# Optimization experiments

Measured on AMD Instinct MI355X. Metric: run time of the kernel, lower is better.

Reference implementation:

```python
import jax, jax.numpy as jnp
import numpy as np

N = 50000
E = 800000
IN_C = 64
HID = 64
HEADS = 4
NUM_GRAPHS = 64
NEG_SLOPE = 0.2


def setup_inputs() -> dict:
    key = jax.random.key(0)
    ks = jax.random.split(key, 16)
    x = jax.random.normal(ks[0], (N, IN_C), dtype=jnp.float32)
    edge_index = jax.random.randint(ks[1], (2, E), 0, N, dtype=jnp.int64)
    batch = jnp.sort(jax.random.randint(ks[2], (N,), 0, NUM_GRAPHS, dtype=jnp.int64))
    s = lambda *sh: 1.0 / np.sqrt(sh[0])
    # conv1: in -> HID per head, concat -> HEADS*HID
    W1 = jax.random.normal(ks[3], (IN_C, HEADS * HID), dtype=jnp.float32) * s(IN_C)
    a1_src = jax.random.normal(ks[4], (HEADS, HID), dtype=jnp.float32) * s(HID)
    a1_dst = jax.random.normal(ks[5], (HEADS, HID), dtype=jnp.float32) * s(HID)
    b1 = jnp.zeros((HEADS * HID,), dtype=jnp.float32)
    # conv2: HEADS*HID -> HID, single head, no concat
    W2 = jax.random.normal(ks[6], (HEADS * HID, HID), dtype=jnp.float32) * s(HEADS * HID)
    a2_src = jax.random.normal(ks[7], (1, HID), dtype=jnp.float32) * s(HID)
    a2_dst = jax.random.normal(ks[8], (1, HID), dtype=jnp.float32) * s(HID)
    b2 = jnp.zeros((HID,), dtype=jnp.float32)
    # MLP head: HID -> 16 -> 1
    Wh1 = jax.random.normal(ks[9], (HID, 16), dtype=jnp.float32) * s(HID)
    bh1 = jnp.zeros((16,), dtype=jnp.float32)
    Wh2 = jax.random.normal(ks[10], (16, 1), dtype=jnp.float32) * s(16)
    bh2 = jnp.zeros((1,), dtype=jnp.float32)
    return {"x": x, "edge_index": edge_index, "batch": batch,
            "W1": W1, "a1_src": a1_src, "a1_dst": a1_dst, "b1": b1,
            "W2": W2, "a2_src": a2_src, "a2_dst": a2_dst, "b2": b2,
            "Wh1": Wh1, "bh1": bh1, "Wh2": Wh2, "bh2": bh2}


def _gat_conv(x, src, dst, W, a_src, a_dst, b, concat):
    """PyG-style GATConv (eval mode, self-loops already appended)."""
    H, C = a_src.shape
    xp = (x @ W).reshape(-1, H, C)                      # [N,H,C]
    e_s = jnp.einsum('nhc,hc->nh', xp, a_src)            # source contribution
    e_d = jnp.einsum('nhc,hc->nh', xp, a_dst)            # target contribution
    e = jax.nn.leaky_relu(e_s[src] + e_d[dst], NEG_SLOPE)  # [E,H]
    # segment softmax over edges grouped by destination node
    m = jax.ops.segment_max(e, dst, num_segments=N)
    ex = jnp.exp(e - m[dst])
    denom = jax.ops.segment_sum(ex, dst, num_segments=N)
    alpha = ex / denom[dst]                              # [E,H]
    out = jax.ops.segment_sum(alpha[:, :, None] * xp[src], dst, num_segments=N)  # [N,H,C]
    out = out.reshape(-1, H * C) if concat else out.mean(axis=1)
    return out + b


def reference(x, edge_index, batch, W1, a1_src, a1_dst, b1,
              W2, a2_src, a2_dst, b2, Wh1, bh1, Wh2, bh2):
    # add self loops once (GATConv default add_self_loops=True)
    loop = jnp.arange(N, dtype=edge_index.dtype)
    src = jnp.concatenate([edge_index[0], loop])
    dst = jnp.concatenate([edge_index[1], loop])
    h = jax.nn.elu(_gat_conv(x, src, dst, W1, a1_src, a1_dst, b1, concat=True))
    h = _gat_conv(h, src, dst, W2, a2_src, a2_dst, b2, concat=False)
    # global mean pool over graphs
    summed = jax.ops.segment_sum(h, batch, num_segments=NUM_GRAPHS)
    cnt = jax.ops.segment_sum(jnp.ones((N,), h.dtype), batch, num_segments=NUM_GRAPHS)
    pooled = summed / jnp.maximum(cnt, 1.0)[:, None]     # [G,HID]
    z = jax.nn.relu(pooled @ Wh1 + bh1)
    out = jax.nn.sigmoid(z @ Wh2 + bh2)
    return out.squeeze(-1)                               # [G]
```

## Files before the change

### kernel.cpp

```cpp
#include <hip/hip_runtime.h>
#include <math.h>

#define N_NODES 50000
#define N_EDGES 800000
#define EA (N_EDGES + N_NODES)
#define HEADS 4
#define HID 64
#define NG 64
#define NEG_SLOPE 0.2f
#define SCAN_CHUNK 1024
#define NBLK ((N_NODES + SCAN_CHUNK - 1) / SCAN_CHUNK)

typedef _Float16 f16x8 __attribute__((ext_vector_type(8)));
typedef float f32x4 __attribute__((ext_vector_type(4)));
struct h4 { _Float16 a, b, c, d; };

__device__ inline float lrelu(float x) { return x > 0.f ? x : NEG_SLOPE * x; }

__device__ inline f16x8 ldfrag(const _Float16* __restrict__ p, int lq) {
    uint2 lo = *(const uint2*)(p + lq * 4);
    uint2 hi = *(const uint2*)(p + 16 + lq * 4);
    union { uint4 u; f16x8 v; } f;
    f.u = make_uint4(lo.x, lo.y, hi.x, hi.y);
    return f.v;
}

__global__ void k_zero(int* __restrict__ deg, float* __restrict__ pooled,
                       float* __restrict__ cnt)
{
    int i = blockIdx.x * 256 + threadIdx.x;
    int st = gridDim.x * 256;
    for (int j = i; j < N_NODES; j += st) deg[j] = 0;
    if (i < NG * HID) pooled[i] = 0.f;
    if (i < NG) cnt[i] = 0.f;
}

__global__ void k_deg(const int* __restrict__ ei, int* __restrict__ deg)
{
    int e = blockIdx.x * 256 + threadIdx.x;
    if (e >= EA) return;
    int d = (e < N_EDGES) ? ei[N_EDGES + e] : e - N_EDGES;
    atomicAdd(&deg[d], 1);
}

__global__ __launch_bounds__(1024) void k_scan1(const int* __restrict__ deg,
        int* __restrict__ incl, int* __restrict__ blksum)
{
    __shared__ int sd[SCAN_CHUNK];
    int t = threadIdx.x;
    int i = blockIdx.x * SCAN_CHUNK + t;
    sd[t] = (i < N_NODES) ? deg[i] : 0;
    for (int off = 1; off < SCAN_CHUNK; off <<= 1) {
        __syncthreads();
        int u = (t >= off) ? sd[t - off] : 0;
        __syncthreads();
        sd[t] += u;
    }
    if (i < N_NODES) incl[i] = sd[t];
    if (t == SCAN_CHUNK - 1) blksum[blockIdx.x] = sd[t];
}

__global__ __launch_bounds__(256) void k_scan2p(const int* __restrict__ blksum,
        int* __restrict__ blkoff, const float* __restrict__ W1,
        const float* __restrict__ a1s, const float* __restrict__ a1d,
        const float* __restrict__ W2, const float* __restrict__ a2s,
        const float* __restrict__ a2d,
        _Float16* __restrict__ W1P, _Float16* __restrict__ W2P,
        float* __restrict__ va1s, float* __restrict__ va1d,
        float* __restrict__ va2s, float* __restrict__ va2d)
{
    const int t = threadIdx.x;
    if (t == 0) {
        int acc = 0;
        for (int b = 0; b < NBLK; ++b) { blkoff[b] = acc; acc += blksum[b]; }
    }
    for (int i = t; i < 256 * 64; i += 256) {
        int np = i >> 6, k = i & 63;
        W1P[i] = (_Float16)W1[k * 256 + (np & 3) * 64 + (np >> 2)];
    }
    for (int i = t; i < 64 * 256; i += 256) {
        int n = i >> 8, k = i & 255;
        W2P[i] = (_Float16)W2[k * 64 + n];
    }
    {
        int k = t >> 2, h = t & 3;
        float ss = 0.f, sd = 0.f;
        for (int c = 0; c < 64; ++c) {
            float wv = W1[k * 256 + h * 64 + c];
            ss = fmaf(wv, a1s[h * 64 + c], ss);
            sd = fmaf(wv, a1d[h * 64 + c], sd);
        }
        va1s[t] = ss;
        va1d[t] = sd;
    }
    {
        float ss = 0.f, sd = 0.f;
        for (int c = 0; c < 64; ++c) {
            float wv = W2[t * 64 + c];
            ss = fmaf(wv, a2s[c], ss);
            sd = fmaf(wv, a2d[c], sd);
        }
        va2s[t] = ss;
        va2d[t] = sd;
    }
}

__global__ void k_scan3(const int* __restrict__ incl, const int* __restrict__ blkoff,
                        const int* __restrict__ deg, const int* __restrict__ batch,
                        int* __restrict__ rowptr, int* __restrict__ cursor,
                        float* __restrict__ cnt)
{
    int i = blockIdx.x * 256 + threadIdx.x;
    bool act = i < N_NODES;
    if (act) {
        int v = incl[i] + blkoff[i >> 10];
        rowptr[i + 1] = v;
        cursor[i] = v - deg[i];
        if (i == 0) rowptr[0] = 0;
    }
    int g = act ? batch[i] : -1;
    int lane = threadIdx.x & 63;
    int g0 = __shfl(g, 0, 64);
    if (__all(g == g0)) {
        if (lane == 0 && g0 >= 0) atomicAdd(&cnt[g0], 64.f);
    } else if (act) {
        atomicAdd(&cnt[g], 1.f);
    }
}

__global__ void k_fill(const int* __restrict__ ei, int* __restrict__ cursor,
                       int* __restrict__ csr_src)
{
    int e = blockIdx.x * 256 + threadIdx.x;
    if (e >= EA) return;
    int s, d;
    if (e < N_EDGES) { s = ei[e]; d = ei[N_EDGES + e]; }
    else { s = e - N_EDGES; d = s; }
    int pos = atomicAdd(&cursor[d], 1);
    csr_src[pos] = s;
}

__global__ __launch_bounds__(256) void k_gemm1(const float* __restrict__ x,
        const _Float16* __restrict__ W1P, const float* __restrict__ va1s,
        const float* __restrict__ va1d, _Float16* __restrict__ xp1h,
        float* __restrict__ e1s, float* __restrict__ e1d)
{
    const int t = threadIdx.x;
    const int lane = t & 63, w = t >> 6;
    const int l15 = lane & 15, lq = lane >> 4;
    const int m0 = blockIdx.x * 64 + w * 16;
    const int mrow = m0 + l15;
    const int mc = mrow < N_NODES ? mrow : N_NODES - 1;
    const float* xr = x + (size_t)mc * 64;
    float4 x0 = *(const float4*)(xr + lq * 4);
    float4 x1 = *(const float4*)(xr + 16 + lq * 4);
    float4 x2 = *(const float4*)(xr + 32 + lq * 4);
    float4 x3 = *(const float4*)(xr + 48 + lq * 4);
    const float4* vs4 = (const float4*)va1s;
    const float4* vd4 = (const float4*)va1d;
    float4 es = {0,0,0,0}, ed = {0,0,0,0};
    {
        float xv[16] = {x0.x,x0.y,x0.z,x0.w, x1.x,x1.y,x1.z,x1.w,
                        x2.x,x2.y,x2.z,x2.w, x3.x,x3.y,x3.z,x3.w};
        #pragma unroll
        for (int q = 0; q < 4; ++q) {
            int kb = q * 16 + lq * 4;
            #pragma unroll
            for (int j = 0; j < 4; ++j) {
                float v = xv[q * 4 + j];
                float4 a = vs4[kb + j], b = vd4[kb + j];
                es.x = fmaf(v, a.x, es.x); es.y = fmaf(v, a.y, es.y);
                es.z = fmaf(v, a.z, es.z); es.w = fmaf(v, a.w, es.w);
                ed.x = fmaf(v, b.x, ed.x); ed.y = fmaf(v, b.y, ed.y);
                ed.z = fmaf(v, b.z, ed.z); ed.w = fmaf(v, b.w, ed.w);
            }
        }
    }
    #pragma unroll
    for (int off = 16; off <= 32; off <<= 1) {
        es.x += __shfl_down(es.x, off, 64); es.y += __shfl_down(es.y, off, 64);
        es.z += __shfl_down(es.z, off, 64); es.w += __shfl_down(es.w, off, 64);
        ed.x += __shfl_down(ed.x, off, 64); ed.y += __shfl_down(ed.y, off, 64);
        ed.z += __shfl_down(ed.z, off, 64); ed.w += __shfl_down(ed.w, off, 64);
    }
    if (lq == 0 && mrow < N_NODES) {
        ((float4*)e1s)[mrow] = es;
        ((float4*)e1d)[mrow] = ed;
    }
    union { f16x8 v; _Float16 e[8]; } u0, u1;
    u0.e[0]=(_Float16)x0.x; u0.e[1]=(_Float16)x0.y; u0.e[2]=(_Float16)x0.z; u0.e[3]=(_Float16)x0.w;
    u0.e[4]=(_Float16)x1.x; u0.e[5]=(_Float16)x1.y; u0.e[6]=(_Float16)x1.z; u0.e[7]=(_Float16)x1.w;
    u1.e[0]=(_Float16)x2.x; u1.e[1]=(_Float16)x2.y; u1.e[2]=(_Float16)x2.z; u1.e[3]=(_Float16)x2.w;
    u1.e[4]=(_Float16)x3.x; u1.e[5]=(_Float16)x3.y; u1.e[6]=(_Float16)x3.z; u1.e[7]=(_Float16)x3.w;
    #pragma unroll
    for (int ct = 0; ct < 16; ++ct) {
        const _Float16* wrow = W1P + (size_t)(ct * 16 + l15) * 64;
        f16x8 wf0 = ldfrag(wrow, lq);
        f16x8 wf1 = ldfrag(wrow + 32, lq);
        f32x4 acc = {0.f, 0.f, 0.f, 0.f};
        acc = __builtin_amdgcn_mfma_f32_16x16x32_f16(wf0, u0.v, acc, 0, 0, 0);
        acc = __builtin_amdgcn_mfma_f32_16x16x32_f16(wf1, u1.v, acc, 0, 0, 0);
        if (mrow < N_NODES) {
            union { uint2 u2; _Float16 e[4]; } o;
            o.e[0]=(_Float16)acc[0]; o.e[1]=(_Float16)acc[1];
            o.e[2]=(_Float16)acc[2]; o.e[3]=(_Float16)acc[3];
            *(uint2*)(xp1h + (size_t)mrow * 256 + ct * 16 + lq * 4) = o.u2;
        }
    }
}

__global__ __launch_bounds__(256) void k_aggr1(const int* __restrict__ rowptr,
        const int* __restrict__ csr_src, const float* __restrict__ e1s,
        const float* __restrict__ e1d, const _Float16* __restrict__ xp1h,
        const float* __restrict__ b1, const float* __restrict__ va2s,
        const float* __restrict__ va2d, _Float16* __restrict__ h1h,
        float* __restrict__ e2s_o, float* __restrict__ e2d_o)
{
    const int lane = threadIdx.x & 63;
    const int w = __builtin_amdgcn_readfirstlane(threadIdx.x >> 6);
    const int d = blockIdx.x * 4 + w;
    if (d >= N_NODES) return;
    const int beg = rowptr[d], end = rowptr[d + 1];
    const float4 edv = ((const float4*)e1d)[d];
    float a0 = 0.f, a1 = 0.f, a2 = 0.f, a3 = 0.f;
    float d0 = 0.f, d1 = 0.f, d2 = 0.f, d3 = 0.f;
    for (int jb = beg; jb < end; jb += 64) {
        int myj = jb + lane;
        int sv = 0;
        float px = 0.f, py = 0.f, pz = 0.f, pw = 0.f;
        if (myj < end) {
            sv = csr_src[myj];
            float4 q = ((const float4*)e1s)[sv];
            px = __expf(lrelu(q.x + edv.x));
            py = __expf(lrelu(q.y + edv.y));
            pz = __expf(lrelu(q.z + edv.z));
            pw = __expf(lrelu(q.w + edv.w));
        }
        int nj = end - jb; if (nj > 64) nj = 64;
        int njr = (nj + 7) & ~7;
        for (int j = 0; j < njr; j += 8) {
            #pragma unroll
            for (int k = 0; k < 8; ++k) {
                int s = __shfl(sv, j + k, 64);
                float p0 = __shfl(px, j + k, 64);
                float p1 = __shfl(py, j + k, 64);
                float p2 = __shfl(pz, j + k, 64);
                float p3 = __shfl(pw, j + k, 64);
                h4 xv = *(const h4*)(xp1h + (size_t)s * 256 + lane * 4);
                a0 = fmaf(p0, (float)xv.a, a0);
                a1 = fmaf(p1, (float)xv.b, a1);
                a2 = fmaf(p2, (float)xv.c, a2);
                a3 = fmaf(p3, (float)xv.d, a3);
                d0 += p0; d1 += p1; d2 += p2; d3 += p3;
            }
        }
    }
    float acc[4] = {a0 / d0, a1 / d1, a2 / d2, a3 / d3};
    float es = 0.f, edd = 0.f;
    #pragma unroll
    for (int hh = 0; hh < 4; ++hh) {
        float v = acc[hh] + b1[hh * 64 + lane];
        v = v > 0.f ? v : __expf(v) - 1.f;
        h1h[(size_t)d * 256 + hh * 64 + lane] = (_Float16)v;
        es  = fmaf(v, va2s[hh * 64 + lane], es);
        edd = fmaf(v, va2d[hh * 64 + lane], edd);
    }
    #pragma unroll
    for (int off = 32; off > 0; off >>= 1) {
        es += __shfl_down(es, off, 64);
        edd += __shfl_down(edd, off, 64);
    }
    if (lane == 0) { e2s_o[d] = es; e2d_o[d] = edd; }
}

__global__ __launch_bounds__(256) void k_gemm2(const _Float16* __restrict__ h1h,
        const _Float16* __restrict__ W2P, _Float16* __restrict__ xp2h)
{
    const int t = threadIdx.x;
    const int lane = t & 63, w = t >> 6;
    const int l15 = lane & 15, lq = lane >> 4;
    const int m0 = blockIdx.x * 64 + w * 16;
    const int mrow = m0 + l15;
    const _Float16* arow = h1h + (size_t)(m0 + l15) * 256;
    f16x8 af[8];
    #pragma unroll
    for (int ks = 0; ks < 8; ++ks) af[ks] = ldfrag(arow + ks * 32, lq);
    #pragma unroll
    for (int ct = 0; ct < 4; ++ct) {
        const _Float16* wrow = W2P + (size_t)(ct * 16 + l15) * 256;
        f32x4 acc = {0.f, 0.f, 0.f, 0.f};
        #pragma unroll
        for (int ks = 0; ks < 8; ++ks) {
            f16x8 wf = ldfrag(wrow + ks * 32, lq);
            acc = __builtin_amdgcn_mfma_f32_16x16x32_f16(wf, af[ks], acc, 0, 0, 0);
        }
        if (mrow < N_NODES) {
            union { uint2 u2; _Float16 e[4]; } o;
            o.e[0]=(_Float16)acc[0]; o.e[1]=(_Float16)acc[1];
            o.e[2]=(_Float16)acc[2]; o.e[3]=(_Float16)acc[3];
            *(uint2*)(xp2h + (size_t)mrow * 64 + ct * 16 + lq * 4) = o.u2;
        }
    }
}

__global__ __launch_bounds__(256) void k_aggr2(const int* __restrict__ rowptr,
        const int* __restrict__ csr_src, const float* __restrict__ e2s,
        const float* __restrict__ e2d, const _Float16* __restrict__ xp2h,
        const float* __restrict__ b2, const int* __restrict__ batch,
        float* __restrict__ pooled)
{
    const int lane = threadIdx.x & 63;
    const int w = __builtin_amdgcn_readfirstlane(threadIdx.x >> 6);
    const int d = blockIdx.x * 4 + w;
    if (d >= N_NODES) return;
    const int beg = rowptr[d], end = rowptr[d + 1];
    const float edv = e2d[d];
    float acc = 0.f, den = 0.f;
    for (int jb = beg; jb < end; jb += 64) {
        int myj = jb + lane;
        int sv = 0;
        float p = 0.f;
        if (myj < end) {
            sv = csr_src[myj];
            p = __expf(lrelu(e2s[sv] + edv));
        }
        int nj = end - jb; if (nj > 64) nj = 64;
        int njr = (nj + 15) & ~15;
        for (int j = 0; j < njr; j += 16) {
            #pragma unroll
            for (int k = 0; k < 16; ++k) {
                int s = __shfl(sv, j + k, 64);
                float pv = __shfl(p, j + k, 64);
                acc = fmaf(pv, (float)xp2h[(size_t)s * 64 + lane], acc);
                den += pv;
            }
        }
    }
    float val = acc / den + b2[lane];
    int g = batch[d];
    atomicAdd(&pooled[g * 64 + lane], val);
}

__global__ void k_mlp(const float* __restrict__ pooled, const float* __restrict__ cnt,
                      const float* __restrict__ Wh1, const float* __restrict__ bh1,
                      const float* __restrict__ Wh2, const float* __restrict__ bh2,
                      float* __restrict__ out)
{
    int g = threadIdx.x;
    float inv = 1.f / fmaxf(cnt[g], 1.f);
    float p[64];
    #pragma unroll
    for (int c = 0; c < 64; ++c) p[c] = pooled[g * 64 + c] * inv;
    float acc2 = bh2[0];
    for (int j = 0; j < 16; ++j) {
        float z = bh1[j];
        #pragma unroll
        for (int c = 0; c < 64; ++c) z = fmaf(p[c], Wh1[c * 16 + j], z);
        z = fmaxf(z, 0.f);
        acc2 = fmaf(z, Wh2[j], acc2);
    }
    out[g] = 1.f / (1.f + expf(-acc2));
}

extern "C" void kernel_launch(void* const* d_in, const int* in_sizes, int n_in,
                              void* d_out, int out_size, void* d_ws, size_t ws_size,
                              hipStream_t stream)
{
    const float* x      = (const float*)d_in[0];
    const int*   ei     = (const int*)d_in[1];
    const int*   batch  = (const int*)d_in[2];
    const float* W1     = (const float*)d_in[3];
    const float* a1s    = (const float*)d_in[4];
    const float* a1d    = (const float*)d_in[5];
    const float* b1     = (const float*)d_in[6];
    const float* W2     = (const float*)d_in[7];
    const float* a2s    = (const float*)d_in[8];
    const float* a2d    = (const float*)d_in[9];
    const float* b2     = (const float*)d_in[10];
    const float* Wh1    = (const float*)d_in[11];
    const float* bh1    = (const float*)d_in[12];
    const float* Wh2    = (const float*)d_in[13];
    const float* bh2    = (const float*)d_in[14];
    float* out = (float*)d_out;

    float* ws = (float*)d_ws;
    size_t off = 0;
    _Float16* xp1h = (_Float16*)(ws + off); off += (size_t)N_NODES * 128;
    _Float16* h1h  = (_Float16*)(ws + off); off += (size_t)(N_NODES + 64) * 128;
    float* e1s    = ws + off; off += (size_t)N_NODES * 4;
    float* e1d    = ws + off; off += (size_t)N_NODES * 4;
    float* e2s    = ws + off; off += N_NODES;
    float* e2d    = ws + off; off += N_NODES;
    _Float16* xp2h = (_Float16*)(ws + off); off += (size_t)N_NODES * 32;
    _Float16* W1P  = (_Float16*)(ws + off); off += 8192;
    _Float16* W2P  = (_Float16*)(ws + off); off += 8192;
    float* va1s   = ws + off; off += 256;
    float* va1d   = ws + off; off += 256;
    float* va2s   = ws + off; off += 256;
    float* va2d   = ws + off; off += 256;
    float* pooled = ws + off; off += NG * HID;
    float* cnt    = ws + off; off += NG;
    int* rowptr   = (int*)(ws + off); off += N_NODES + 2;
    int* cursor   = (int*)(ws + off); off += N_NODES;
    int* csr_src  = (int*)(ws + off); off += EA;
    int* blksum   = (int*)(ws + off); off += NBLK;
    int* blkoff   = (int*)(ws + off); off += NBLK;
    int* deg  = (int*)h1h;
    int* incl = deg + N_NODES;

    const int BE = (EA + 255) / 256;
    const int BN = (N_NODES + 255) / 256;
    const int BW = (N_NODES + 3) / 4;
    const int BG = (N_NODES + 63) / 64;

    hipLaunchKernelGGL(k_zero,   dim3(64),   dim3(256),  0, stream, deg, pooled, cnt);
    hipLaunchKernelGGL(k_deg,    dim3(BE),   dim3(256),  0, stream, ei, deg);
    hipLaunchKernelGGL(k_scan1,  dim3(NBLK), dim3(1024), 0, stream, deg, incl, blksum);
    hipLaunchKernelGGL(k_scan2p, dim3(1),    dim3(256),  0, stream,
                       blksum, blkoff, W1, a1s, a1d, W2, a2s, a2d,
                       W1P, W2P, va1s, va1d, va2s, va2d);
    hipLaunchKernelGGL(k_scan3,  dim3(BN),   dim3(256),  0, stream,
                       incl, blkoff, deg, batch, rowptr, cursor, cnt);
    hipLaunchKernelGGL(k_fill,   dim3(BE),   dim3(256),  0, stream, ei, cursor, csr_src);

    hipLaunchKernelGGL(k_gemm1,  dim3(BG),   dim3(256),  0, stream,
                       x, W1P, va1s, va1d, xp1h, e1s, e1d);
    hipLaunchKernelGGL(k_aggr1,  dim3(BW),   dim3(256),  0, stream,
                       rowptr, csr_src, e1s, e1d, xp1h, b1, va2s, va2d,
                       h1h, e2s, e2d);
    hipLaunchKernelGGL(k_gemm2,  dim3(BG),   dim3(256),  0, stream, h1h, W2P, xp2h);
    hipLaunchKernelGGL(k_aggr2,  dim3(BW),   dim3(256),  0, stream,
                       rowptr, csr_src, e2s, e2d, xp2h, b2, batch, pooled);

    hipLaunchKernelGGL(k_mlp, dim3(1), dim3(64), 0, stream,
                       pooled, cnt, Wh1, bh1, Wh2, bh2, out);
}
```

Before: 434.2 us.

## Aggregate raw features before the layer-1 projection to shrink the gather width

```diff
diff --git a/kernel.cpp b/kernel.cpp
--- a/kernel.cpp
+++ b/kernel.cpp
@@ -13,7 +13,6 @@
 
 typedef _Float16 f16x8 __attribute__((ext_vector_type(8)));
 typedef float f32x4 __attribute__((ext_vector_type(4)));
-struct h4 { _Float16 a, b, c, d; };
 
 __device__ inline float lrelu(float x) { return x > 0.f ? x : NEG_SLOPE * x; }
 
@@ -65,7 +64,7 @@
         const float* __restrict__ a1s, const float* __restrict__ a1d,
         const float* __restrict__ W2, const float* __restrict__ a2s,
         const float* __restrict__ a2d,
-        _Float16* __restrict__ W1P, _Float16* __restrict__ W2P,
+        _Float16* __restrict__ W1T, _Float16* __restrict__ W2P,
         float* __restrict__ va1s, float* __restrict__ va1d,
         float* __restrict__ va2s, float* __restrict__ va2d)
 {
@@ -75,8 +74,8 @@
         for (int b = 0; b < NBLK; ++b) { blkoff[b] = acc; acc += blksum[b]; }
     }
     for (int i = t; i < 256 * 64; i += 256) {
-        int np = i >> 6, k = i & 63;
-        W1P[i] = (_Float16)W1[k * 256 + (np & 3) * 64 + (np >> 2)];
+        int n = i >> 6, k = i & 63;
+        W1T[i] = (_Float16)W1[k * 256 + n];
     }
     for (int i = t; i < 64 * 256; i += 256) {
         int n = i >> 8, k = i & 255;
@@ -140,81 +139,37 @@
     csr_src[pos] = s;
 }
 
-__global__ __launch_bounds__(256) void k_gemm1(const float* __restrict__ x,
-        const _Float16* __restrict__ W1P, const float* __restrict__ va1s,
-        const float* __restrict__ va1d, _Float16* __restrict__ xp1h,
-        float* __restrict__ e1s, float* __restrict__ e1d)
-{
-    const int t = threadIdx.x;
-    const int lane = t & 63, w = t >> 6;
-    const int l15 = lane & 15, lq = lane >> 4;
-    const int m0 = blockIdx.x * 64 + w * 16;
-    const int mrow = m0 + l15;
-    const int mc = mrow < N_NODES ? mrow : N_NODES - 1;
-    const float* xr = x + (size_t)mc * 64;
-    float4 x0 = *(const float4*)(xr + lq * 4);
-    float4 x1 = *(const float4*)(xr + 16 + lq * 4);
-    float4 x2 = *(const float4*)(xr + 32 + lq * 4);
-    float4 x3 = *(const float4*)(xr + 48 + lq * 4);
-    const float4* vs4 = (const float4*)va1s;
-    const float4* vd4 = (const float4*)va1d;
-    float4 es = {0,0,0,0}, ed = {0,0,0,0};
-    {
-        float xv[16] = {x0.x,x0.y,x0.z,x0.w, x1.x,x1.y,x1.z,x1.w,
-                        x2.x,x2.y,x2.z,x2.w, x3.x,x3.y,x3.z,x3.w};
-        #pragma unroll
-        for (int q = 0; q < 4; ++q) {
-            int kb = q * 16 + lq * 4;
-            #pragma unroll
-            for (int j = 0; j < 4; ++j) {
-                float v = xv[q * 4 + j];
-                float4 a = vs4[kb + j], b = vd4[kb + j];
-                es.x = fmaf(v, a.x, es.x); es.y = fmaf(v, a.y, es.y);
-                es.z = fmaf(v, a.z, es.z); es.w = fmaf(v, a.w, es.w);
-                ed.x = fmaf(v, b.x, ed.x); ed.y = fmaf(v, b.y, ed.y);
-                ed.z = fmaf(v, b.z, ed.z); ed.w = fmaf(v, b.w, ed.w);
-            }
-        }
-    }
-    #pragma unroll
-    for (int off = 16; off <= 32; off <<= 1) {
-        es.x += __shfl_down(es.x, off, 64); es.y += __shfl_down(es.y, off, 64);
-        es.z += __shfl_down(es.z, off, 64); es.w += __shfl_down(es.w, off, 64);
-        ed.x += __shfl_down(ed.x, off, 64); ed.y += __shfl_down(ed.y, off, 64);
-        ed.z += __shfl_down(ed.z, off, 64); ed.w += __shfl_down(ed.w, off, 64);
-    }
-    if (lq == 0 && mrow < N_NODES) {
-        ((float4*)e1s)[mrow] = es;
-        ((float4*)e1d)[mrow] = ed;
-    }
-    union { f16x8 v; _Float16 e[8]; } u0, u1;
-    u0.e[0]=(_Float16)x0.x; u0.e[1]=(_Float16)x0.y; u0.e[2]=(_Float16)x0.z; u0.e[3]=(_Float16)x0.w;
-    u0.e[4]=(_Float16)x1.x; u0.e[5]=(_Float16)x1.y; u0.e[6]=(_Float16)x1.z; u0.e[7]=(_Float16)x1.w;
-    u1.e[0]=(_Float16)x2.x; u1.e[1]=(_Float16)x2.y; u1.e[2]=(_Float16)x2.z; u1.e[3]=(_Float16)x2.w;
-    u1.e[4]=(_Float16)x3.x; u1.e[5]=(_Float16)x3.y; u1.e[6]=(_Float16)x3.z; u1.e[7]=(_Float16)x3.w;
-    #pragma unroll
-    for (int ct = 0; ct < 16; ++ct) {
-        const _Float16* wrow = W1P + (size_t)(ct * 16 + l15) * 64;
-        f16x8 wf0 = ldfrag(wrow, lq);
-        f16x8 wf1 = ldfrag(wrow + 32, lq);
-        f32x4 acc = {0.f, 0.f, 0.f, 0.f};
-        acc = __builtin_amdgcn_mfma_f32_16x16x32_f16(wf0, u0.v, acc, 0, 0, 0);
-        acc = __builtin_amdgcn_mfma_f32_16x16x32_f16(wf1, u1.v, acc, 0, 0, 0);
-        if (mrow < N_NODES) {
-            union { uint2 u2; _Float16 e[4]; } o;
-            o.e[0]=(_Float16)acc[0]; o.e[1]=(_Float16)acc[1];
-            o.e[2]=(_Float16)acc[2]; o.e[3]=(_Float16)acc[3];
-            *(uint2*)(xp1h + (size_t)mrow * 256 + ct * 16 + lq * 4) = o.u2;
-        }
+__global__ __launch_bounds__(256) void k_prep(const float* __restrict__ x,
+        const float* __restrict__ va1s, const float* __restrict__ va1d,
+        _Float16* __restrict__ xh, float* __restrict__ e1s, float* __restrict__ e1d)
+{
+    const int lane = threadIdx.x & 63;
+    const int w = threadIdx.x >> 6;
+    const int n = blockIdx.x * 4 + w;
+    if (n >= N_NODES) return;
+    float xv = x[(size_t)n * 64 + lane];
+    xh[(size_t)n * 64 + lane] = (_Float16)xv;
+    float4 vs = ((const float4*)va1s)[lane];
+    float4 vd = ((const float4*)va1d)[lane];
+    float s0 = xv * vs.x, s1 = xv * vs.y, s2 = xv * vs.z, s3 = xv * vs.w;
+    float d0 = xv * vd.x, d1 = xv * vd.y, d2 = xv * vd.z, d3 = xv * vd.w;
+    #pragma unroll
+    for (int off = 32; off > 0; off >>= 1) {
+        s0 += __shfl_down(s0, off, 64); s1 += __shfl_down(s1, off, 64);
+        s2 += __shfl_down(s2, off, 64); s3 += __shfl_down(s3, off, 64);
+        d0 += __shfl_down(d0, off, 64); d1 += __shfl_down(d1, off, 64);
+        d2 += __shfl_down(d2, off, 64); d3 += __shfl_down(d3, off, 64);
+    }
+    if (lane == 0) {
+        ((float4*)e1s)[n] = make_float4(s0, s1, s2, s3);
+        ((float4*)e1d)[n] = make_float4(d0, d1, d2, d3);
     }
 }
 
 __global__ __launch_bounds__(256) void k_aggr1(const int* __restrict__ rowptr,
         const int* __restrict__ csr_src, const float* __restrict__ e1s,
-        const float* __restrict__ e1d, const _Float16* __restrict__ xp1h,
-        const float* __restrict__ b1, const float* __restrict__ va2s,
-        const float* __restrict__ va2d, _Float16* __restrict__ h1h,
-        float* __restrict__ e2s_o, float* __restrict__ e2d_o)
+        const float* __restrict__ e1d, const _Float16* __restrict__ xh,
+        _Float16* __restrict__ agg)
 {
     const int lane = threadIdx.x & 63;
     const int w = __builtin_amdgcn_readfirstlane(threadIdx.x >> 6);
@@ -237,40 +192,81 @@
             pw = __expf(lrelu(q.w + edv.w));
         }
         int nj = end - jb; if (nj > 64) nj = 64;
-        int njr = (nj + 7) & ~7;
-        for (int j = 0; j < njr; j += 8) {
+        int njr = (nj + 15) & ~15;
+        for (int j = 0; j < njr; j += 16) {
             #pragma unroll
-            for (int k = 0; k < 8; ++k) {
+            for (int k = 0; k < 16; ++k) {
                 int s = __shfl(sv, j + k, 64);
                 float p0 = __shfl(px, j + k, 64);
                 float p1 = __shfl(py, j + k, 64);
                 float p2 = __shfl(pz, j + k, 64);
                 float p3 = __shfl(pw, j + k, 64);
-                h4 xv = *(const h4*)(xp1h + (size_t)s * 256 + lane * 4);
-                a0 = fmaf(p0, (float)xv.a, a0);
-                a1 = fmaf(p1, (float)xv.b, a1);
-                a2 = fmaf(p2, (float)xv.c, a2);
-                a3 = fmaf(p3, (float)xv.d, a3);
+                float xv = (float)xh[(size_t)s * 64 + lane];
+                a0 = fmaf(p0, xv, a0);
+                a1 = fmaf(p1, xv, a1);
+                a2 = fmaf(p2, xv, a2);
+                a3 = fmaf(p3, xv, a3);
                 d0 += p0; d1 += p1; d2 += p2; d3 += p3;
             }
         }
     }
-    float acc[4] = {a0 / d0, a1 / d1, a2 / d2, a3 / d3};
+    _Float16* ad = agg + (size_t)d * 256;
+    ad[lane]        = (_Float16)(a0 / d0);
+    ad[64 + lane]   = (_Float16)(a1 / d1);
+    ad[128 + lane]  = (_Float16)(a2 / d2);
+    ad[192 + lane]  = (_Float16)(a3 / d3);
+}
+
+__global__ __launch_bounds__(256) void k_post1(const _Float16* __restrict__ agg,
+        const _Float16* __restrict__ W1T, const float* __restrict__ b1,
+        const float* __restrict__ va2s, const float* __restrict__ va2d,
+        _Float16* __restrict__ h1h, float* __restrict__ e2s_o,
+        float* __restrict__ e2d_o)
+{
+    const int t = threadIdx.x;
+    const int lane = t & 63, w = t >> 6;
+    const int l15 = lane & 15, lq = lane >> 4;
+    const int m0 = blockIdx.x * 64 + w * 16;
+    const int mrow = m0 + l15;
+    const int mc = mrow < N_NODES ? mrow : N_NODES - 1;
+    const _Float16* arow = agg + (size_t)mc * 256;
+    f16x8 af[8];
+    #pragma unroll
+    for (int ks = 0; ks < 8; ++ks) af[ks] = ldfrag(arow + ks * 32, lq);
     float es = 0.f, edd = 0.f;
     #pragma unroll
-    for (int hh = 0; hh < 4; ++hh) {
-        float v = acc[hh] + b1[hh * 64 + lane];
-        v = v > 0.f ? v : __expf(v) - 1.f;
-        h1h[(size_t)d * 256 + hh * 64 + lane] = (_Float16)v;
-        es  = fmaf(v, va2s[hh * 64 + lane], es);
-        edd = fmaf(v, va2d[hh * 64 + lane], edd);
-    }
-    #pragma unroll
-    for (int off = 32; off > 0; off >>= 1) {
-        es += __shfl_down(es, off, 64);
+    for (int ct = 0; ct < 16; ++ct) {
+        const int hh = ct >> 2;
+        const _Float16* wrow = W1T + (size_t)(ct * 16 + l15) * 64;
+        f16x8 wf0 = ldfrag(wrow, lq);
+        f16x8 wf1 = ldfrag(wrow + 32, lq);
+        f32x4 acc = {0.f, 0.f, 0.f, 0.f};
+        acc = __builtin_amdgcn_mfma_f32_16x16x32_f16(wf0, af[2 * hh], acc, 0, 0, 0);
+        acc = __builtin_amdgcn_mfma_f32_16x16x32_f16(wf1, af[2 * hh + 1], acc, 0, 0, 0);
+        float4 bb = ((const float4*)b1)[ct * 4 + lq];
+        float4 ssv = ((const float4*)va2s)[ct * 4 + lq];
+        float4 ddv = ((const float4*)va2d)[ct * 4 + lq];
+        float bbv[4] = {bb.x, bb.y, bb.z, bb.w};
+        float sss[4] = {ssv.x, ssv.y, ssv.z, ssv.w};
+        float ddd[4] = {ddv.x, ddv.y, ddv.z, ddv.w};
+        union { uint2 u2; _Float16 e[4]; } o;
+        #pragma unroll
+        for (int j = 0; j < 4; ++j) {
+            float v = acc[j] + bbv[j];
+            v = v > 0.f ? v : __expf(v) - 1.f;
+            o.e[j] = (_Float16)v;
+            es  = fmaf(v, sss[j], es);
+            edd = fmaf(v, ddd[j], edd);
+        }
+        if (mrow < N_NODES)
+            *(uint2*)(h1h + (size_t)mrow * 256 + ct * 16 + lq * 4) = o.u2;
+    }
+    #pragma unroll
+    for (int off = 16; off <= 32; off <<= 1) {
+        es  += __shfl_down(es, off, 64);
         edd += __shfl_down(edd, off, 64);
     }
-    if (lane == 0) { e2s_o[d] = es; e2d_o[d] = edd; }
+    if (lq == 0 && mrow < N_NODES) { e2s_o[mrow] = es; e2d_o[mrow] = edd; }
 }
 
 __global__ __launch_bounds__(256) void k_gemm2(const _Float16* __restrict__ h1h,
@@ -385,14 +381,15 @@
 
     float* ws = (float*)d_ws;
     size_t off = 0;
-    _Float16* xp1h = (_Float16*)(ws + off); off += (size_t)N_NODES * 128;
+    _Float16* xh   = (_Float16*)(ws + off); off += (size_t)N_NODES * 32;
+    _Float16* agg  = (_Float16*)(ws + off); off += (size_t)(N_NODES + 64) * 128;
     _Float16* h1h  = (_Float16*)(ws + off); off += (size_t)(N_NODES + 64) * 128;
     float* e1s    = ws + off; off += (size_t)N_NODES * 4;
     float* e1d    = ws + off; off += (size_t)N_NODES * 4;
     float* e2s    = ws + off; off += N_NODES;
     float* e2d    = ws + off; off += N_NODES;
     _Float16* xp2h = (_Float16*)(ws + off); off += (size_t)N_NODES * 32;
-    _Float16* W1P  = (_Float16*)(ws + off); off += 8192;
+    _Float16* W1T  = (_Float16*)(ws + off); off += 8192;
     _Float16* W2P  = (_Float16*)(ws + off); off += 8192;
     float* va1s   = ws + off; off += 256;
     float* va1d   = ws + off; off += 256;
@@ -405,7 +402,7 @@
     int* csr_src  = (int*)(ws + off); off += EA;
     int* blksum   = (int*)(ws + off); off += NBLK;
     int* blkoff   = (int*)(ws + off); off += NBLK;
-    int* deg  = (int*)h1h;
+    int* deg  = (int*)agg;
     int* incl = deg + N_NODES;
 
     const int BE = (EA + 255) / 256;
@@ -418,16 +415,17 @@
     hipLaunchKernelGGL(k_scan1,  dim3(NBLK), dim3(1024), 0, stream, deg, incl, blksum);
     hipLaunchKernelGGL(k_scan2p, dim3(1),    dim3(256),  0, stream,
                        blksum, blkoff, W1, a1s, a1d, W2, a2s, a2d,
-                       W1P, W2P, va1s, va1d, va2s, va2d);
+                       W1T, W2P, va1s, va1d, va2s, va2d);
     hipLaunchKernelGGL(k_scan3,  dim3(BN),   dim3(256),  0, stream,
                        incl, blkoff, deg, batch, rowptr, cursor, cnt);
     hipLaunchKernelGGL(k_fill,   dim3(BE),   dim3(256),  0, stream, ei, cursor, csr_src);
 
-    hipLaunchKernelGGL(k_gemm1,  dim3(BG),   dim3(256),  0, stream,
-                       x, W1P, va1s, va1d, xp1h, e1s, e1d);
+    hipLaunchKernelGGL(k_prep,   dim3(BW),   dim3(256),  0, stream,
+                       x, va1s, va1d, xh, e1s, e1d);
     hipLaunchKernelGGL(k_aggr1,  dim3(BW),   dim3(256),  0, stream,
-                       rowptr, csr_src, e1s, e1d, xp1h, b1, va2s, va2d,
-                       h1h, e2s, e2d);
+                       rowptr, csr_src, e1s, e1d, xh, agg);
+    hipLaunchKernelGGL(k_post1,  dim3(BG),   dim3(256),  0, stream,
+                       agg, W1T, b1, va2s, va2d, h1h, e2s, e2d);
     hipLaunchKernelGGL(k_gemm2,  dim3(BG),   dim3(256),  0, stream, h1h, W2P, xp2h);
     hipLaunchKernelGGL(k_aggr2,  dim3(BW),   dim3(256),  0, stream,
                        rowptr, csr_src, e2s, e2d, xp2h, b2, batch, pooled);
```

Measured after the change: 476.1 us. 1.1x slower.
